# Kernel tuning notes

Hardware: AMD Instinct MI355X
Metric: run time of the kernel (lower is better)

## Reference

```python
import jax, jax.numpy as jnp
import numpy as np

N_NODES = 8192
N_FEAT = 256
N_EDGES = 131072
K = 4


def setup_inputs() -> dict:
    key = jax.random.key(0)
    k1, k2, k3 = jax.random.split(key, 3)
    x = jax.random.normal(k1, (N_NODES, N_FEAT), dtype=jnp.float32)
    edge_index = jax.random.randint(k2, (2, N_EDGES), 0, N_NODES, dtype=jnp.int64)
    edge_weight = jax.random.uniform(k3, (N_EDGES,), dtype=jnp.float32)
    return {"k": K, "x": x, "edge_index": edge_index, "edge_weight": edge_weight}


def reference(k, x, edge_index, edge_weight):
    n = x.shape[0]
    src, dst = edge_index[0], edge_index[1]
    # Symmetrized dense adjacency, matching the torch loop:
    #   adj[src, dst] = w  then  adj[dst, src] += w
    adj = jnp.zeros((n, n), dtype=x.dtype)
    adj = adj.at[src, dst].set(edge_weight)
    adj = adj.at[dst, src].add(edge_weight)
    # M = [I | A | A^2 | ... | A^{k-1}] (N x kN) times block_diag(x,...,x)
    # (kN x kF) is exactly concat([A^j @ x for j in 0..k-1], axis=1) -- we
    # compute that directly and never form the block-diagonal zeros.
    outs = [x]
    h = x
    for _ in range(1, k):
        h = adj @ h  # A^j @ x  (A symmetric, so order is immaterial)
        outs.append(h)
    return jnp.concatenate(outs, axis=1)  # [N, k*F]
```

## Files before the change

### kernel.cpp

```cpp
#include <hip/hip_runtime.h>

#define N_NODES 8192
#define N_FEAT  256
#define N_EDGES 131072
#define KPOW    4
#define OUT_LD  1024
#define RCAP    128
#define COL_MASK 8191u

typedef float    f32x4 __attribute__((ext_vector_type(4)));
typedef unsigned u32x4 __attribute__((ext_vector_type(4)));
typedef unsigned u32x2 __attribute__((ext_vector_type(2)));

static __device__ __forceinline__ float bflo(unsigned u) {
    union { unsigned i; float f; } v; v.i = u << 16; return v.f;
}
static __device__ __forceinline__ float bfhi(unsigned u) {
    union { unsigned i; float f; } v; v.i = u & 0xffff0000u; return v.f;
}
static __device__ __forceinline__ unsigned short f2bf(float f) {
    union { float f; unsigned i; } v = { f };
    return (unsigned short)((v.i + 0x7fffu + ((v.i >> 16) & 1u)) >> 16);
}

__global__ void k_scatter_copy(const int* __restrict__ ei, const float* __restrict__ ew,
                               int* __restrict__ len, u32x2* __restrict__ ent,
                               const float* __restrict__ x, float* __restrict__ out,
                               unsigned short* __restrict__ xb) {
    if (blockIdx.x < 2048) {
        int t = blockIdx.x * blockDim.x + threadIdx.x;
        int row = t >> 6;
        int lane = t & 63;
        f32x4 v = __builtin_nontemporal_load(
            (const f32x4*)(x + (size_t)row * N_FEAT + lane * 4));
        __builtin_nontemporal_store(v, (f32x4*)(out + (size_t)row * OUT_LD + lane * 4));
        ushort4 b;
        b.x = f2bf(v.x); b.y = f2bf(v.y); b.z = f2bf(v.z); b.w = f2bf(v.w);
        *(ushort4*)(xb + (size_t)row * N_FEAT + lane * 4) = b;
    } else {
        int e = (blockIdx.x - 2048) * blockDim.x + threadIdx.x;
        if (e >= N_EDGES) return;
        int src = __builtin_nontemporal_load(ei + e);
        int dst = __builtin_nontemporal_load(ei + N_EDGES + e);
        unsigned wbits = __float_as_uint(__builtin_nontemporal_load(ew + e));
        int s0 = atomicAdd(&len[dst], 1);
        if (s0 < RCAP) {
            u32x2 v; v.x = (unsigned)src; v.y = wbits;
            __builtin_nontemporal_store(v, ent + (size_t)dst * RCAP + s0);
        }
        int s1 = atomicAdd(&len[src], 1);
        if (s1 < RCAP) {
            u32x2 v; v.x = (1u << 30) | ((unsigned)e << 13) | (unsigned)dst; v.y = wbits;
            __builtin_nontemporal_store(v, ent + (size_t)src * RCAP + s1);
        }
    }
}

__global__ __launch_bounds__(256) void k_dedup(const int* __restrict__ len,
                                               unsigned* __restrict__ entw) {
    int lane = threadIdx.x & 63;
    int row = blockIdx.x * 4 + (threadIdx.x >> 6);
    int n = __builtin_amdgcn_readfirstlane(len[row]);
    if (n > RCAP) n = RCAP;
    size_t base = (size_t)row * RCAP;
    unsigned v0 = __builtin_nontemporal_load(entw + 2 * (base + lane));
    unsigned v1 = __builtin_nontemporal_load(entw + 2 * (base + 64 + lane));
    bool k0 = false, k1 = false;
    int j0 = n < 64 ? n : 64;
    for (int j = 0; j < j0; ++j) {
        unsigned b = (unsigned)__shfl((int)v0, j);
        if (b >> 30) {
            k0 |= (((b ^ v0) & COL_MASK) == 0u) && (b > v0);
            k1 |= (((b ^ v1) & COL_MASK) == 0u) && (b > v1);
        }
    }
    for (int j = 0; j < n - 64; ++j) {
        unsigned b = (unsigned)__shfl((int)v1, j);
        if (b >> 30) {
            k0 |= (((b ^ v0) & COL_MASK) == 0u) && (b > v0);
            k1 |= (((b ^ v1) & COL_MASK) == 0u) && (b > v1);
        }
    }
    int ngs = 8 * ((n + 7) >> 3);
    int s1 = 64 + lane;
    if (lane < n) { if (k0 && (v0 >> 30)) entw[2 * (base + lane) + 1] = 0u; }
    else if (lane < ngs) entw[2 * (base + lane) + 1] = 0u;
    if (s1 < n) { if (k1 && (v1 >> 30)) entw[2 * (base + s1) + 1] = 0u; }
    else if (s1 < ngs) entw[2 * (base + s1) + 1] = 0u;
}

__global__ __launch_bounds__(256) void k_spmm(const int* __restrict__ len,
                                              const u32x2* __restrict__ ent,
                                              const unsigned short* __restrict__ hinb,
                                              float* __restrict__ hout,
                                              unsigned short* __restrict__ houtb,
                                              int write_bf) {
    int lane = threadIdx.x & 63;
    int row = __builtin_amdgcn_readfirstlane(blockIdx.x * 4 + (threadIdx.x >> 6));
    int n = len[row];
    if (n > RCAP) n = RCAP;
    const u32x4* e4 = (const u32x4*)(ent + (size_t)row * RCAP);
    float ax = 0.f, ay = 0.f, az = 0.f, aw = 0.f;
    int ng = (n + 7) >> 3;

    u32x4 q0, q1, q2, q3;
    if (ng > 0) {
        q0 = __builtin_nontemporal_load(e4 + 0);
        q1 = __builtin_nontemporal_load(e4 + 1);
        q2 = __builtin_nontemporal_load(e4 + 2);
        q3 = __builtin_nontemporal_load(e4 + 3);
    }
    for (int g = 0; g < ng; ++g) {
        int gp = (g + 1 < 16) ? (g + 1) : 0;
        u32x4 p0 = __builtin_nontemporal_load(e4 + gp * 4 + 0);
        u32x4 p1 = __builtin_nontemporal_load(e4 + gp * 4 + 1);
        u32x4 p2 = __builtin_nontemporal_load(e4 + gp * 4 + 2);
        u32x4 p3 = __builtin_nontemporal_load(e4 + gp * 4 + 3);
        u32x4 qq[4] = { q0, q1, q2, q3 };
#pragma unroll
        for (int k = 0; k < 4; ++k) {
            unsigned ca = qq[k].x & COL_MASK; float wa = __uint_as_float(qq[k].y);
            unsigned cb = qq[k].z & COL_MASK; float wb = __uint_as_float(qq[k].w);
            uint2 ua = *(const uint2*)(hinb + (size_t)ca * N_FEAT + lane * 4);
            uint2 ub = *(const uint2*)(hinb + (size_t)cb * N_FEAT + lane * 4);
            ax += wa * bflo(ua.x); ay += wa * bfhi(ua.x);
            az += wa * bflo(ua.y); aw += wa * bfhi(ua.y);
            ax += wb * bflo(ub.x); ay += wb * bfhi(ub.x);
            az += wb * bflo(ub.y); aw += wb * bfhi(ub.y);
        }
        q0 = p0; q1 = p1; q2 = p2; q3 = p3;
    }

    f32x4 r; r.x = ax; r.y = ay; r.z = az; r.w = aw;
    __builtin_nontemporal_store(r, (f32x4*)(hout + (size_t)row * OUT_LD + lane * 4));
    if (write_bf) {
        ushort4 b;
        b.x = f2bf(ax); b.y = f2bf(ay); b.z = f2bf(az); b.w = f2bf(aw);
        *(ushort4*)(houtb + (size_t)row * N_FEAT + lane * 4) = b;
    }
}

extern "C" void kernel_launch(void* const* d_in, const int* in_sizes, int n_in,
                              void* d_out, int out_size, void* d_ws, size_t ws_size,
                              hipStream_t stream) {
    const float* x  = (const float*)d_in[1];
    const int*   ei = (const int*)d_in[2];
    const float* ew = (const float*)d_in[3];
    float* out = (float*)d_out;

    int* len   = (int*)d_ws;
    u32x2* ent = (u32x2*)(len + N_NODES);
    unsigned short* hb0 = (unsigned short*)(ent + (size_t)N_NODES * RCAP);
    unsigned short* hb1 = hb0 + (size_t)N_NODES * N_FEAT;
    unsigned short* hb2 = hb1 + (size_t)N_NODES * N_FEAT;

    (void)hipMemsetAsync(len, 0, (size_t)N_NODES * sizeof(int), stream);

    const int TB = 256;
    const int EB = N_EDGES / TB;

    k_scatter_copy<<<2048 + EB, TB, 0, stream>>>(ei, ew, len, ent, x, out, hb0);
    k_dedup<<<N_NODES / 4, TB, 0, stream>>>(len, (unsigned*)ent);

    const unsigned short* hin = hb0;
    for (int j = 1; j < KPOW; ++j) {
        float* hout = out + (size_t)j * N_FEAT;
        unsigned short* houtb = (j == 1) ? hb1 : hb2;
        int write_bf = (j < KPOW - 1) ? 1 : 0;
        k_spmm<<<N_NODES / 4, TB, 0, stream>>>(len, ent, hin, hout, houtb, write_bf);
        hin = houtb;
    }
}
```

Measured before the change: 146.3 us.

## Split SpMM feature dimension across two blocks per row group

Each row's 256-feature output is now split into two halves handled by separate blocks, doubling the grid, and each lane handles 2 features instead of 4. Block indices are interleaved so both halves of a row group are launched close together, which should let them share the edge-list reads in cache. Gather loads are issued all up front before the FMAs so more memory requests are in flight. In exchange, edge list and length reads are duplicated across the two blocks and each gather load is narrower (4 bytes per lane instead of 8).

```diff
diff --git a/kernel.cpp b/kernel.cpp
--- a/kernel.cpp
+++ b/kernel.cpp
@@ -9,6 +9,7 @@
 #define COL_MASK 8191u
 
 typedef float    f32x4 __attribute__((ext_vector_type(4)));
+typedef float    f32x2 __attribute__((ext_vector_type(2)));
 typedef unsigned u32x4 __attribute__((ext_vector_type(4)));
 typedef unsigned u32x2 __attribute__((ext_vector_type(2)));
 
@@ -96,11 +97,15 @@
                                               unsigned short* __restrict__ houtb,
                                               int write_bf) {
     int lane = threadIdx.x & 63;
-    int row = __builtin_amdgcn_readfirstlane(blockIdx.x * 4 + (threadIdx.x >> 6));
+    int b = blockIdx.x;
+    int half = (b >> 2) & 1;
+    int rb = (b >> 3) * 4 + (b & 3);
+    int row = __builtin_amdgcn_readfirstlane(rb * 4 + (threadIdx.x >> 6));
     int n = len[row];
     if (n > RCAP) n = RCAP;
     const u32x4* e4 = (const u32x4*)(ent + (size_t)row * RCAP);
-    float ax = 0.f, ay = 0.f, az = 0.f, aw = 0.f;
+    const unsigned short* hbase = hinb + half * 128 + lane * 2;
+    float ax = 0.f, ay = 0.f;
     int ng = (n + 7) >> 3;
 
     u32x4 q0, q1, q2, q3;
@@ -117,26 +122,28 @@
         u32x4 p2 = __builtin_nontemporal_load(e4 + gp * 4 + 2);
         u32x4 p3 = __builtin_nontemporal_load(e4 + gp * 4 + 3);
         u32x4 qq[4] = { q0, q1, q2, q3 };
+        unsigned ua[8]; float wa[8];
 #pragma unroll
         for (int k = 0; k < 4; ++k) {
-            unsigned ca = qq[k].x & COL_MASK; float wa = __uint_as_float(qq[k].y);
-            unsigned cb = qq[k].z & COL_MASK; float wb = __uint_as_float(qq[k].w);
-            uint2 ua = *(const uint2*)(hinb + (size_t)ca * N_FEAT + lane * 4);
-            uint2 ub = *(const uint2*)(hinb + (size_t)cb * N_FEAT + lane * 4);
-            ax += wa * bflo(ua.x); ay += wa * bfhi(ua.x);
-            az += wa * bflo(ua.y); aw += wa * bfhi(ua.y);
-            ax += wb * bflo(ub.x); ay += wb * bfhi(ub.x);
-            az += wb * bflo(ub.y); aw += wb * bfhi(ub.y);
+            unsigned ca = qq[k].x & COL_MASK; wa[2 * k] = __uint_as_float(qq[k].y);
+            unsigned cb = qq[k].z & COL_MASK; wa[2 * k + 1] = __uint_as_float(qq[k].w);
+            ua[2 * k]     = *(const unsigned*)(hbase + (size_t)ca * N_FEAT);
+            ua[2 * k + 1] = *(const unsigned*)(hbase + (size_t)cb * N_FEAT);
+        }
+#pragma unroll
+        for (int k = 0; k < 8; ++k) {
+            ax += wa[k] * bflo(ua[k]);
+            ay += wa[k] * bfhi(ua[k]);
         }
         q0 = p0; q1 = p1; q2 = p2; q3 = p3;
     }
 
-    f32x4 r; r.x = ax; r.y = ay; r.z = az; r.w = aw;
-    __builtin_nontemporal_store(r, (f32x4*)(hout + (size_t)row * OUT_LD + lane * 4));
+    f32x2 r; r.x = ax; r.y = ay;
+    __builtin_nontemporal_store(r,
+        (f32x2*)(hout + (size_t)row * OUT_LD + half * 128 + lane * 2));
     if (write_bf) {
-        ushort4 b;
-        b.x = f2bf(ax); b.y = f2bf(ay); b.z = f2bf(az); b.w = f2bf(aw);
-        *(ushort4*)(houtb + (size_t)row * N_FEAT + lane * 4) = b;
+        unsigned packed = ((unsigned)f2bf(ay) << 16) | (unsigned)f2bf(ax);
+        *(unsigned*)(houtb + (size_t)row * N_FEAT + half * 128 + lane * 2) = packed;
     }
 }
 
@@ -167,7 +174,7 @@
         float* hout = out + (size_t)j * N_FEAT;
         unsigned short* houtb = (j == 1) ? hb1 : hb2;
         int write_bf = (j < KPOW - 1) ? 1 : 0;
-        k_spmm<<<N_NODES / 4, TB, 0, stream>>>(len, ent, hin, hout, houtb, write_bf);
+        k_spmm<<<2 * N_NODES / 4, TB, 0, stream>>>(len, ent, hin, hout, houtb, write_bf);
         hin = houtb;
     }
 }
```

Measured after the change: 143.8 us. No clear change (-1.7%).

## Stage row entries in LDS and split wave into two half-waves gathering 16B rows

Applied to the files above, without the earlier changes.

The SpMM kernel now copies each row's neighbour list into shared memory, then has each half-wave handle alternate edges while every lane gathers 16 bytes (8 bf16 features) per neighbour row. Eight gathers are issued before any accumulation, and the two halves are combined with a cross-half shuffle, after which one half writes the fp32 output and the other the bf16 copy. Dedup padding is widened to groups of 16 to match. Nontemporal hints are dropped across the kernels. The aim is wider, more parallel gathers and more memory-level parallelism, at the cost of LDS use and extra shuffle work.

```diff
diff --git a/kernel.cpp b/kernel.cpp
--- a/kernel.cpp
+++ b/kernel.cpp
@@ -31,27 +31,27 @@
         int t = blockIdx.x * blockDim.x + threadIdx.x;
         int row = t >> 6;
         int lane = t & 63;
-        f32x4 v = __builtin_nontemporal_load(
-            (const f32x4*)(x + (size_t)row * N_FEAT + lane * 4));
-        __builtin_nontemporal_store(v, (f32x4*)(out + (size_t)row * OUT_LD + lane * 4));
-        ushort4 b;
-        b.x = f2bf(v.x); b.y = f2bf(v.y); b.z = f2bf(v.z); b.w = f2bf(v.w);
-        *(ushort4*)(xb + (size_t)row * N_FEAT + lane * 4) = b;
+        f32x4 v = *(const f32x4*)(x + (size_t)row * N_FEAT + lane * 4);
+        *(f32x4*)(out + (size_t)row * OUT_LD + lane * 4) = v;
+        u32x2 pb;
+        pb.x = ((unsigned)f2bf(v.y) << 16) | f2bf(v.x);
+        pb.y = ((unsigned)f2bf(v.w) << 16) | f2bf(v.z);
+        *(u32x2*)(xb + (size_t)row * N_FEAT + lane * 4) = pb;
     } else {
         int e = (blockIdx.x - 2048) * blockDim.x + threadIdx.x;
         if (e >= N_EDGES) return;
-        int src = __builtin_nontemporal_load(ei + e);
-        int dst = __builtin_nontemporal_load(ei + N_EDGES + e);
-        unsigned wbits = __float_as_uint(__builtin_nontemporal_load(ew + e));
+        int src = ei[e];
+        int dst = ei[N_EDGES + e];
+        unsigned wbits = __float_as_uint(ew[e]);
         int s0 = atomicAdd(&len[dst], 1);
         if (s0 < RCAP) {
             u32x2 v; v.x = (unsigned)src; v.y = wbits;
-            __builtin_nontemporal_store(v, ent + (size_t)dst * RCAP + s0);
+            ent[(size_t)dst * RCAP + s0] = v;
         }
         int s1 = atomicAdd(&len[src], 1);
         if (s1 < RCAP) {
             u32x2 v; v.x = (1u << 30) | ((unsigned)e << 13) | (unsigned)dst; v.y = wbits;
-            __builtin_nontemporal_store(v, ent + (size_t)src * RCAP + s1);
+            ent[(size_t)src * RCAP + s1] = v;
         }
     }
 }
@@ -63,8 +63,8 @@
     int n = __builtin_amdgcn_readfirstlane(len[row]);
     if (n > RCAP) n = RCAP;
     size_t base = (size_t)row * RCAP;
-    unsigned v0 = __builtin_nontemporal_load(entw + 2 * (base + lane));
-    unsigned v1 = __builtin_nontemporal_load(entw + 2 * (base + 64 + lane));
+    unsigned v0 = entw[2 * (base + lane)];
+    unsigned v1 = entw[2 * (base + 64 + lane)];
     bool k0 = false, k1 = false;
     int j0 = n < 64 ? n : 64;
     for (int j = 0; j < j0; ++j) {
@@ -81,7 +81,7 @@
             k1 |= (((b ^ v1) & COL_MASK) == 0u) && (b > v1);
         }
     }
-    int ngs = 8 * ((n + 7) >> 3);
+    int ngs = 16 * ((n + 15) >> 4);
     int s1 = 64 + lane;
     if (lane < n) { if (k0 && (v0 >> 30)) entw[2 * (base + lane) + 1] = 0u; }
     else if (lane < ngs) entw[2 * (base + lane) + 1] = 0u;
@@ -95,48 +95,62 @@
                                               float* __restrict__ hout,
                                               unsigned short* __restrict__ houtb,
                                               int write_bf) {
+    __shared__ u32x2 sent[4 * RCAP];
+    int wave = threadIdx.x >> 6;
     int lane = threadIdx.x & 63;
-    int row = __builtin_amdgcn_readfirstlane(blockIdx.x * 4 + (threadIdx.x >> 6));
-    int n = len[row];
+    int row = blockIdx.x * 4 + wave;
+    int n = __builtin_amdgcn_readfirstlane(len[row]);
     if (n > RCAP) n = RCAP;
-    const u32x4* e4 = (const u32x4*)(ent + (size_t)row * RCAP);
-    float ax = 0.f, ay = 0.f, az = 0.f, aw = 0.f;
-    int ng = (n + 7) >> 3;
 
-    u32x4 q0, q1, q2, q3;
-    if (ng > 0) {
-        q0 = __builtin_nontemporal_load(e4 + 0);
-        q1 = __builtin_nontemporal_load(e4 + 1);
-        q2 = __builtin_nontemporal_load(e4 + 2);
-        q3 = __builtin_nontemporal_load(e4 + 3);
-    }
+    const u32x2* ep = ent + (size_t)row * RCAP;
+    u32x2* sp = sent + wave * RCAP;
+    sp[lane] = ep[lane];
+    sp[lane + 64] = ep[lane + 64];
+    __builtin_amdgcn_s_waitcnt(0);
+
+    int half = lane >> 5;
+    int fl   = lane & 31;
+    const unsigned short* hbase = hinb + fl * 8;
+    float a0 = 0.f, a1 = 0.f, a2 = 0.f, a3 = 0.f,
+          a4 = 0.f, a5 = 0.f, a6 = 0.f, a7 = 0.f;
+    int ng = (n + 15) >> 4;
+
     for (int g = 0; g < ng; ++g) {
-        int gp = (g + 1 < 16) ? (g + 1) : 0;
-        u32x4 p0 = __builtin_nontemporal_load(e4 + gp * 4 + 0);
-        u32x4 p1 = __builtin_nontemporal_load(e4 + gp * 4 + 1);
-        u32x4 p2 = __builtin_nontemporal_load(e4 + gp * 4 + 2);
-        u32x4 p3 = __builtin_nontemporal_load(e4 + gp * 4 + 3);
-        u32x4 qq[4] = { q0, q1, q2, q3 };
+        const u32x2* ge = sp + g * 16 + half;
+        u32x4 us[8];
 #pragma unroll
-        for (int k = 0; k < 4; ++k) {
-            unsigned ca = qq[k].x & COL_MASK; float wa = __uint_as_float(qq[k].y);
-            unsigned cb = qq[k].z & COL_MASK; float wb = __uint_as_float(qq[k].w);
-            uint2 ua = *(const uint2*)(hinb + (size_t)ca * N_FEAT + lane * 4);
-            uint2 ub = *(const uint2*)(hinb + (size_t)cb * N_FEAT + lane * 4);
-            ax += wa * bflo(ua.x); ay += wa * bfhi(ua.x);
-            az += wa * bflo(ua.y); aw += wa * bfhi(ua.y);
-            ax += wb * bflo(ub.x); ay += wb * bfhi(ub.x);
-            az += wb * bflo(ub.y); aw += wb * bfhi(ub.y);
+        for (int t = 0; t < 8; ++t) {
+            unsigned c = ge[2 * t].x & COL_MASK;
+            us[t] = *(const u32x4*)(hbase + (size_t)c * N_FEAT);
         }
-        q0 = p0; q1 = p1; q2 = p2; q3 = p3;
+#pragma unroll
+        for (int t = 0; t < 8; ++t) {
+            float w = __uint_as_float(ge[2 * t].y);
+            a0 += w * bflo(us[t].x); a1 += w * bfhi(us[t].x);
+            a2 += w * bflo(us[t].y); a3 += w * bfhi(us[t].y);
+            a4 += w * bflo(us[t].z); a5 += w * bfhi(us[t].z);
+            a6 += w * bflo(us[t].w); a7 += w * bfhi(us[t].w);
+        }
     }
 
-    f32x4 r; r.x = ax; r.y = ay; r.z = az; r.w = aw;
-    __builtin_nontemporal_store(r, (f32x4*)(hout + (size_t)row * OUT_LD + lane * 4));
-    if (write_bf) {
-        ushort4 b;
-        b.x = f2bf(ax); b.y = f2bf(ay); b.z = f2bf(az); b.w = f2bf(aw);
-        *(ushort4*)(houtb + (size_t)row * N_FEAT + lane * 4) = b;
+    a0 += __shfl_xor(a0, 32); a1 += __shfl_xor(a1, 32);
+    a2 += __shfl_xor(a2, 32); a3 += __shfl_xor(a3, 32);
+    a4 += __shfl_xor(a4, 32); a5 += __shfl_xor(a5, 32);
+    a6 += __shfl_xor(a6, 32); a7 += __shfl_xor(a7, 32);
+
+    if (half == 0) {
+        float* op = hout + (size_t)row * OUT_LD + fl * 8;
+        f32x4 r0; r0.x = a0; r0.y = a1; r0.z = a2; r0.w = a3;
+        f32x4 r1; r1.x = a4; r1.y = a5; r1.z = a6; r1.w = a7;
+        *(f32x4*)op = r0;
+        *(f32x4*)(op + 4) = r1;
+    } else if (write_bf) {
+        u32x4 pb;
+        pb.x = ((unsigned)f2bf(a1) << 16) | f2bf(a0);
+        pb.y = ((unsigned)f2bf(a3) << 16) | f2bf(a2);
+        pb.z = ((unsigned)f2bf(a5) << 16) | f2bf(a4);
+        pb.w = ((unsigned)f2bf(a7) << 16) | f2bf(a6);
+        *(u32x4*)(houtb + (size_t)row * N_FEAT + fl * 8) = pb;
     }
 }
 
```

Measured after the change: 140.3 us. 1.04x faster.
